# Kernel tuning notes

Measured on AMD Instinct MI355X. Metric: run time of the kernel, lower is better.

## Reference

```python
import jax, jax.numpy as jnp
import numpy as np

N = 100000
E = 1600000
IN_CH = 128
HID = 32
HEADS = 4
OUT_CH = 64
NEG_SLOPE = 0.2


def _gat_conv(x, src, dst, W, att_src, att_dst, bias, heads, out_ch):
    # PyG GATConv (concat=True, add_self_loops handled by caller via src/dst)
    n = x.shape[0]
    xp = (x @ W).reshape(n, heads, out_ch)                  # [N,H,C]
    a_src = (xp * att_src).sum(-1)                          # [N,H]
    a_dst = (xp * att_dst).sum(-1)                          # [N,H]
    e = jax.nn.leaky_relu(a_src[src] + a_dst[dst], NEG_SLOPE)  # [E,H]
    m = jax.ops.segment_max(e, dst, num_segments=n)         # per-dst max (safe: self-loops)
    ex = jnp.exp(e - m[dst])
    denom = jax.ops.segment_sum(ex, dst, num_segments=n)
    alpha = ex / denom[dst]                                  # [E,H]
    out = jax.ops.segment_sum(xp[src] * alpha[:, :, None], dst, num_segments=n)
    return out.reshape(n, heads * out_ch) + bias


def setup_inputs() -> dict:
    key = jax.random.key(0)
    ks = jax.random.split(key, 12)
    sc1 = 1.0 / np.sqrt(IN_CH)
    sc2 = 1.0 / np.sqrt(HID * HEADS * 2)
    return {
        "x_ppi": jax.random.normal(ks[0], (N, IN_CH), jnp.float32),
        "x_go": jax.random.normal(ks[1], (N, IN_CH), jnp.float32),
        "edge_index": jax.random.randint(ks[2], (2, E), 0, N, jnp.int32),
        "W1": jax.random.normal(ks[3], (IN_CH, HEADS * HID), jnp.float32) * sc1,
        "att_src1": jax.random.normal(ks[4], (HEADS, HID), jnp.float32) * sc1,
        "att_dst1": jax.random.normal(ks[5], (HEADS, HID), jnp.float32) * sc1,
        "b1": jnp.zeros((HEADS * HID,), jnp.float32),
        "W2": jax.random.normal(ks[6], (HID * HEADS * 2, OUT_CH), jnp.float32) * sc2,
        "att_src2": jax.random.normal(ks[7], (1, OUT_CH), jnp.float32) * sc2,
        "att_dst2": jax.random.normal(ks[8], (1, OUT_CH), jnp.float32) * sc2,
        "b2": jnp.zeros((OUT_CH,), jnp.float32),
    }


def reference(x_ppi, x_go, edge_index, W1, att_src1, att_dst1, b1, W2, att_src2, att_dst2, b2):
    loops = jnp.arange(N, dtype=edge_index.dtype)
    src = jnp.concatenate([edge_index[0], loops])
    dst = jnp.concatenate([edge_index[1], loops])
    h_ppi = _gat_conv(x_ppi, src, dst, W1, att_src1, att_dst1, b1, HEADS, HID)
    h_go = _gat_conv(x_go, src, dst, W1, att_src1, att_dst1, b1, HEADS, HID)
    h = jax.nn.relu(jnp.concatenate([h_ppi, h_go], axis=-1))  # [N, 2*H*HID]
    out = _gat_conv(h, src, dst, W2, att_src2, att_dst2, b2, 1, OUT_CH)
    return out
```

## Files before the change

kernel.cpp:

```cpp
#include <hip/hip_runtime.h>
#include <hip/hip_fp16.h>

constexpr int NN = 100000;
constexpr int EE = 1600000;
constexpr int ET = EE + NN;
constexpr int EQ = EE / 4;
constexpr int TQ = ET / 4;
constexpr int NBUK = (NN + 255) / 256;
constexpr int PB = 416;
constexpr int GB = (NN + 127) / 128;
constexpr float NEG = 0.2f;

typedef _Float16 f16x8 __attribute__((ext_vector_type(8)));
typedef float    f32x4 __attribute__((ext_vector_type(4)));

__global__ __launch_bounds__(256) void k_wprep0(const float* __restrict__ W1, const float* __restrict__ W2,
                                                _Float16* __restrict__ w1T, _Float16* __restrict__ w2T,
                                                int* __restrict__ bucketCount) {
    if (blockIdx.x == 0) {
        for (int i = threadIdx.x; i < NBUK; i += 256) bucketCount[i] = 0;
    }
    int idx = blockIdx.x * 256 + threadIdx.x;
    if (idx < 128 * 128) {
        int nn = idx >> 7, k = idx & 127;
        w1T[idx] = (_Float16)W1[k * 128 + nn];
    }
    int i2 = idx - 128 * 128;
    if (i2 >= 0 && i2 < 64 * 256) {
        int nn = i2 >> 8, k = i2 & 255;
        w2T[i2] = (_Float16)W2[k * 64 + nn];
    }
}

template <int K, int C, bool SRCF32, int AMODE, int OUTM, int SET>
__device__ __forceinline__ void gemm_dev(int bx, const void* __restrict__ xv,
                                         const _Float16* __restrict__ wT,
                                         const float* __restrict__ as_w, const float* __restrict__ ad_w,
                                         __half* __restrict__ xp,
                                         float* __restrict__ att_s, float* __restrict__ att_d, int n) {
    constexpr int NT = C / 16;
    const int tid  = threadIdx.x;
    const int w    = tid >> 6;
    const int lane = tid & 63;
    const int quad = lane >> 4;
    const int l16  = lane & 15;
    const long r0  = (long)bx * 128;
    const long row0 = r0 + w * 32 + l16;
    const long row1 = row0 + 16;

    f32x4 acc[2][NT];
#pragma unroll
    for (int s = 0; s < 2; s++)
#pragma unroll
        for (int t = 0; t < NT; t++) acc[s][t] = (f32x4){0.f, 0.f, 0.f, 0.f};

#pragma unroll
    for (int ks = 0; ks < K; ks += 32) {
        f16x8 a0 = (f16x8){0, 0, 0, 0, 0, 0, 0, 0};
        f16x8 a1 = (f16x8){0, 0, 0, 0, 0, 0, 0, 0};
        if (SRCF32) {
            if (row0 < n) {
                const float4* p = (const float4*)((const float*)xv + row0 * K + ks) + quad * 2;
                float4 u = p[0], v = p[1];
                a0 = (f16x8){(_Float16)u.x, (_Float16)u.y, (_Float16)u.z, (_Float16)u.w,
                             (_Float16)v.x, (_Float16)v.y, (_Float16)v.z, (_Float16)v.w};
            }
            if (row1 < n) {
                const float4* p = (const float4*)((const float*)xv + row1 * K + ks) + quad * 2;
                float4 u = p[0], v = p[1];
                a1 = (f16x8){(_Float16)u.x, (_Float16)u.y, (_Float16)u.z, (_Float16)u.w,
                             (_Float16)v.x, (_Float16)v.y, (_Float16)v.z, (_Float16)v.w};
            }
        } else {
            if (row0 < n) a0 = *(const f16x8*)((const _Float16*)xv + row0 * K + ks + quad * 8);
            if (row1 < n) a1 = *(const f16x8*)((const _Float16*)xv + row1 * K + ks + quad * 8);
        }
#pragma unroll
        for (int t = 0; t < NT; t++) {
            f16x8 b = *(const f16x8*)(wT + (long)(t * 16 + l16) * K + ks + quad * 8);
            acc[0][t] = __builtin_amdgcn_mfma_f32_16x16x32_f16(a0, b, acc[0][t], 0, 0, 0);
            acc[1][t] = __builtin_amdgcn_mfma_f32_16x16x32_f16(a1, b, acc[1][t], 0, 0, 0);
        }
    }

#pragma unroll
    for (int sub = 0; sub < 2; sub++) {
        long rb = r0 + w * 32 + sub * 16 + quad * 4;
#pragma unroll
        for (int t = 0; t < NT; t++) {
            int c = t * 16 + l16;
#pragma unroll
            for (int rg = 0; rg < 4; rg++) {
                long row = rb + rg;
                if (row < n) {
                    __half hv = __float2half(acc[sub][t][rg]);
                    if (OUTM == 0)
                        xp[row * 256 + ((c >> 1) << 2) + (c & 1) + SET * 2] = hv;
                    else
                        xp[row * (long)C + c] = hv;
                }
            }
        }
    }

    if (AMODE == 1) {
        float asw[8], adw[8];
#pragma unroll
        for (int t = 0; t < 8; t++) {
            int ci = (t >> 1) * 32 + (t & 1) * 16 + l16;
            asw[t] = as_w[ci];
            adw[t] = ad_w[ci];
        }
#pragma unroll
        for (int sub = 0; sub < 2; sub++) {
#pragma unroll
            for (int rg = 0; rg < 4; rg++) {
                long row = r0 + w * 32 + sub * 16 + quad * 4 + rg;
                float hs[4] = {0.f, 0.f, 0.f, 0.f};
                float hd[4] = {0.f, 0.f, 0.f, 0.f};
#pragma unroll
                for (int t = 0; t < 8; t++) {
                    float av = acc[sub][t][rg];
                    hs[t >> 1] += av * asw[t];
                    hd[t >> 1] += av * adw[t];
                }
#pragma unroll
                for (int h = 0; h < 4; h++) {
                    hs[h] += __shfl_xor(hs[h], 1); hs[h] += __shfl_xor(hs[h], 2);
                    hs[h] += __shfl_xor(hs[h], 4); hs[h] += __shfl_xor(hs[h], 8);
                    hd[h] += __shfl_xor(hd[h], 1); hd[h] += __shfl_xor(hd[h], 2);
                    hd[h] += __shfl_xor(hd[h], 4); hd[h] += __shfl_xor(hd[h], 8);
                }
                if (l16 == 0 && row < n) {
#pragma unroll
                    for (int h = 0; h < 4; h++) {
                        att_s[row * 8 + h * 2 + SET] = hs[h];
                        att_d[row * 8 + h * 2 + SET] = hd[h];
                    }
                }
            }
        }
    }
    if (AMODE == 2) {
        float asw[NT], adw[NT];
#pragma unroll
        for (int t = 0; t < NT; t++) {
            asw[t] = as_w[t * 16 + l16];
            adw[t] = ad_w[t * 16 + l16];
        }
#pragma unroll
        for (int sub = 0; sub < 2; sub++) {
#pragma unroll
            for (int rg = 0; rg < 4; rg++) {
                long row = r0 + w * 32 + sub * 16 + quad * 4 + rg;
                float s = 0.f, d = 0.f;
#pragma unroll
                for (int t = 0; t < NT; t++) {
                    float av = acc[sub][t][rg];
                    s += av * asw[t];
                    d += av * adw[t];
                }
                s += __shfl_xor(s, 1); s += __shfl_xor(s, 2); s += __shfl_xor(s, 4); s += __shfl_xor(s, 8);
                d += __shfl_xor(d, 1); d += __shfl_xor(d, 2); d += __shfl_xor(d, 4); d += __shfl_xor(d, 8);
                if (l16 == 0 && row < n) {
                    att_s[row] = s;
                    att_d[row] = d;
                }
            }
        }
    }
}

__device__ __forceinline__ void bcount_dev(int bx, const int4* __restrict__ dst4v,
                                           int* __restrict__ bucketCount) {
    __shared__ int bh[NBUK];
    for (int i = threadIdx.x; i < NBUK; i += 256) bh[i] = 0;
    __syncthreads();
    int gtid = bx * 256 + threadIdx.x;
    for (int q = gtid; q < TQ; q += PB * 256) {
        int4 d;
        if (q < EQ) {
            d = dst4v[q];
        } else {
            int s0 = (q - EQ) * 4;
            d.x = s0; d.y = s0 + 1; d.z = s0 + 2; d.w = s0 + 3;
        }
        atomicAdd(&bh[d.x >> 8], 1);
        atomicAdd(&bh[d.y >> 8], 1);
        atomicAdd(&bh[d.z >> 8], 1);
        atomicAdd(&bh[d.w >> 8], 1);
    }
    __syncthreads();
    for (int i = threadIdx.x; i < NBUK; i += 256)
        if (bh[i]) atomicAdd(&bucketCount[i], bh[i]);
}

__global__ __launch_bounds__(256) void megaA(const float* __restrict__ x_ppi, const float* __restrict__ x_go,
                                             const int4* __restrict__ dst4v,
                                             const _Float16* __restrict__ w1T,
                                             const float* __restrict__ as1, const float* __restrict__ ad1,
                                             __half* __restrict__ xpc,
                                             float* __restrict__ att1s, float* __restrict__ att1d,
                                             int* __restrict__ bucketCount) {
    int bx = blockIdx.x;
    if (bx < GB) {
        gemm_dev<128, 128, true, 1, 0, 0>(bx, x_ppi, w1T, as1, ad1, xpc, att1s, att1d, NN);
    } else if (bx < 2 * GB) {
        gemm_dev<128, 128, true, 1, 0, 1>(bx - GB, x_go, w1T, as1, ad1, xpc, att1s, att1d, NN);
    } else {
        bcount_dev(bx - 2 * GB, dst4v, bucketCount);
    }
}

__global__ __launch_bounds__(256) void gemm_k2(const __half* __restrict__ hbuf,
                                               const _Float16* __restrict__ w2T,
                                               const float* __restrict__ as2, const float* __restrict__ ad2,
                                               __half* __restrict__ xp2,
                                               float* __restrict__ asr2, float* __restrict__ ads2) {
    gemm_dev<256, 64, false, 2, 1, 0>(blockIdx.x, hbuf, w2T, as2, ad2, xp2, asr2, ads2, NN);
}

__global__ __launch_bounds__(512) void k_bscan(const int* __restrict__ bucketCount,
                                               int* __restrict__ bstart, int* __restrict__ gcur,
                                               int* __restrict__ rs) {
    __shared__ int sh[512];
    int t = threadIdx.x;
    int v = (t < NBUK) ? bucketCount[t] : 0;
    sh[t] = v;
    __syncthreads();
    for (int o = 1; o < 512; o <<= 1) {
        int u = (t >= o) ? sh[t - o] : 0;
        __syncthreads();
        sh[t] += u;
        __syncthreads();
    }
    if (t < NBUK) { bstart[t] = sh[t] - v; gcur[t] = sh[t] - v; }
    if (t == 0) { bstart[NBUK] = ET; rs[NN] = ET; }
}

__global__ __launch_bounds__(256) void k_bplace(const int4* __restrict__ src4v, const int4* __restrict__ dst4v,
                                                int* __restrict__ gcur, unsigned int* __restrict__ ebuf) {
    __shared__ int bh[NBUK];
    __shared__ int bbase[NBUK];
    for (int i = threadIdx.x; i < NBUK; i += 256) bh[i] = 0;
    __syncthreads();
    int gtid = blockIdx.x * 256 + threadIdx.x;

    int esrc[16];
    int emeta[16];
#pragma unroll
    for (int it = 0; it < 4; it++) {
        int q = gtid + it * (PB * 256);
        bool valid = q < TQ;
        int4 s, d;
        if (valid) {
            if (q < EQ) { s = src4v[q]; d = dst4v[q]; }
            else { int s0 = (q - EQ) * 4; s.x = s0; s.y = s0 + 1; s.z = s0 + 2; s.w = s0 + 3; d = s; }
        } else {
            s.x = s.y = s.z = s.w = 0; d = s;
        }
        int ss[4] = {s.x, s.y, s.z, s.w};
        int dd[4] = {d.x, d.y, d.z, d.w};
#pragma unroll
        for (int k = 0; k < 4; k++) {
            int idx = it * 4 + k;
            if (valid) {
                int b = dd[k] >> 8, l = dd[k] & 255;
                int r = atomicAdd(&bh[b], 1);
                esrc[idx]  = ss[k];
                emeta[idx] = (b << 21) | (l << 13) | r;
            } else {
                emeta[idx] = -1;
            }
        }
    }
    __syncthreads();
    for (int i = threadIdx.x; i < NBUK; i += 256)
        bbase[i] = bh[i] ? atomicAdd(&gcur[i], bh[i]) : 0;
    __syncthreads();
#pragma unroll
    for (int e = 0; e < 16; e++) {
        int me = emeta[e];
        if (me >= 0) {
            int b = me >> 21, l = (me >> 13) & 255, r = me & 8191;
            ebuf[bbase[b] + r] = ((unsigned)l << 24) | (unsigned)esrc[e];
        }
    }
}

__global__ __launch_bounds__(256) void k_csr(const unsigned int* __restrict__ ebuf,
                                             const int* __restrict__ bstart,
                                             int* __restrict__ rs, int* __restrict__ csr) {
    __shared__ int hist[256];
    __shared__ int sh[256];
    __shared__ int cur[256];
    int b = blockIdx.x;
    int t = threadIdx.x;
    int e0 = bstart[b], e1 = bstart[b + 1];
    hist[t] = 0;
    __syncthreads();
    for (int j = e0 + t; j < e1; j += 256)
        atomicAdd(&hist[ebuf[j] >> 24], 1);
    __syncthreads();
    int v = hist[t];
    sh[t] = v;
    __syncthreads();
    for (int o = 1; o < 256; o <<= 1) {
        int u = (t >= o) ? sh[t - o] : 0;
        __syncthreads();
        sh[t] += u;
        __syncthreads();
    }
    int excl = sh[t] - v;
    cur[t] = excl;
    int v0 = b * 256;
    if (v0 + t < NN) rs[v0 + t] = e0 + excl;
    __syncthreads();
    for (int j = e0 + t; j < e1; j += 256) {
        unsigned int e = ebuf[j];
        int l = (int)(e >> 24);
        int r = atomicAdd(&cur[l], 1);
        csr[e0 + r] = (int)(e & 0x00FFFFFFu);
    }
}

__global__ __launch_bounds__(256) void conv1_packed(const int* __restrict__ rs, const int* __restrict__ csr,
                                                    const uint4* __restrict__ xpc,
                                                    const float2* __restrict__ att_s,
                                                    const float2* __restrict__ att_d,
                                                    const float* __restrict__ bias,
                                                    __half* __restrict__ out) {
    int v = blockIdx.x * 4 + (threadIdx.x >> 6);
    if (v >= NN) return;
    int lane = threadIdx.x & 63;
    int h = lane >> 5;
    int m = lane & 31;
    int hd = m >> 3;
    int e0 = rs[v], e1 = rs[v + 1];

    float2 ad = att_d[v * 4 + hd];
    auto lrexp = [](float e) { e = (e > 0.f) ? e : NEG * e; return __expf(e); };

    float ap0 = 0.f, ap1 = 0.f, ap2 = 0.f, ap3 = 0.f;
    float ag0 = 0.f, ag1 = 0.f, ag2 = 0.f, ag3 = 0.f;
    float dp = 0.f, dg = 0.f;

    int j = e0;
    for (; j + 8 <= e1; j += 8) {
        int s[4]; float2 av[4]; uint4 r[4];
#pragma unroll
        for (int q = 0; q < 4; q++) s[q] = csr[j + 2 * q + h];
#pragma unroll
        for (int q = 0; q < 4; q++) av[q] = att_s[s[q] * 4 + hd];
#pragma unroll
        for (int q = 0; q < 4; q++) r[q] = xpc[(long)s[q] * 32 + m];
#pragma unroll
        for (int q = 0; q < 4; q++) {
            float wx = lrexp(av[q].x + ad.x);
            float wy = lrexp(av[q].y + ad.y);
            dp += wx; dg += wy;
            float2 p01 = __half22float2(*(__half2*)&r[q].x);
            float2 g01 = __half22float2(*(__half2*)&r[q].y);
            float2 p23 = __half22float2(*(__half2*)&r[q].z);
            float2 g23 = __half22float2(*(__half2*)&r[q].w);
            ap0 += wx * p01.x; ap1 += wx * p01.y; ap2 += wx * p23.x; ap3 += wx * p23.y;
            ag0 += wy * g01.x; ag1 += wy * g01.y; ag2 += wy * g23.x; ag3 += wy * g23.y;
        }
    }
    for (; j < e1; j += 2) {
        int jj = j + h;
        int jc = (jj < e1) ? jj : (e1 - 1);
        bool ok = jj < e1;
        int s = csr[jc];
        float2 av = att_s[s * 4 + hd];
        uint4 r = xpc[(long)s * 32 + m];
        float wx = ok ? lrexp(av.x + ad.x) : 0.f;
        float wy = ok ? lrexp(av.y + ad.y) : 0.f;
        dp += wx; dg += wy;
        float2 p01 = __half22float2(*(__half2*)&r.x);
        float2 g01 = __half22float2(*(__half2*)&r.y);
        float2 p23 = __half22float2(*(__half2*)&r.z);
        float2 g23 = __half22float2(*(__half2*)&r.w);
        ap0 += wx * p01.x; ap1 += wx * p01.y; ap2 += wx * p23.x; ap3 += wx * p23.y;
        ag0 += wy * g01.x; ag1 += wy * g01.y; ag2 += wy * g23.x; ag3 += wy * g23.y;
    }

    ap0 += __shfl_xor(ap0, 32); ap1 += __shfl_xor(ap1, 32);
    ap2 += __shfl_xor(ap2, 32); ap3 += __shfl_xor(ap3, 32);
    ag0 += __shfl_xor(ag0, 32); ag1 += __shfl_xor(ag1, 32);
    ag2 += __shfl_xor(ag2, 32); ag3 += __shfl_xor(ag3, 32);
    dp  += __shfl_xor(dp, 32);  dg  += __shfl_xor(dg, 32);

    float ivp = 1.0f / dp, ivg = 1.0f / dg;
    int c0 = 4 * m;
    float4 b4 = *(const float4*)&bias[c0];
    float inv = h ? ivg : ivp;
    float a0 = h ? ag0 : ap0;
    float a1 = h ? ag1 : ap1;
    float a2 = h ? ag2 : ap2;
    float a3 = h ? ag3 : ap3;
    __half2 o01 = __floats2half2_rn(fmaxf(a0 * inv + b4.x, 0.f), fmaxf(a1 * inv + b4.y, 0.f));
    __half2 o23 = __floats2half2_rn(fmaxf(a2 * inv + b4.z, 0.f), fmaxf(a3 * inv + b4.w, 0.f));
    uint2 st;
    st.x = *(unsigned int*)&o01;
    st.y = *(unsigned int*)&o23;
    *(uint2*)(out + (long)v * 256 + h * 128 + c0) = st;
}

__global__ __launch_bounds__(256) void conv2_edge(const int* __restrict__ rs, const int* __restrict__ csr,
                                                  const __half* __restrict__ xp,
                                                  const float* __restrict__ asrc,
                                                  const float* __restrict__ adst,
                                                  const float* __restrict__ bias,
                                                  float* __restrict__ out) {
    int v = blockIdx.x * 4 + (threadIdx.x >> 6);
    if (v >= NN) return;
    int lane = threadIdx.x & 63;
    int qw = lane >> 4;
    int m = lane & 15;
    int e0 = rs[v], e1 = rs[v + 1];
    const uint2* xp2 = (const uint2*)xp;

    float adv = adst[v];
    auto lrexp = [](float e) { e = (e > 0.f) ? e : NEG * e; return __expf(e); };

    float a0 = 0.f, a1 = 0.f, a2 = 0.f, a3 = 0.f, d = 0.f;

    int j = e0;
    for (; j + 16 <= e1; j += 16) {
        int s[4]; float av[4]; uint2 r[4];
#pragma unroll
        for (int k = 0; k < 4; k++) s[k] = csr[j + 4 * k + qw];
#pragma unroll
        for (int k = 0; k < 4; k++) av[k] = asrc[s[k]];
#pragma unroll
        for (int k = 0; k < 4; k++) r[k] = xp2[(long)s[k] * 16 + m];
#pragma unroll
        for (int k = 0; k < 4; k++) {
            float w = lrexp(av[k] + adv);
            d += w;
            float2 x01 = __half22float2(*(__half2*)&r[k].x);
            float2 x23 = __half22float2(*(__half2*)&r[k].y);
            a0 += w * x01.x; a1 += w * x01.y;
            a2 += w * x23.x; a3 += w * x23.y;
        }
    }
    for (; j < e1; j += 4) {
        int jj = j + qw;
        int jc = (jj < e1) ? jj : (e1 - 1);
        int s = csr[jc];
        float av = asrc[s];
        uint2 r = xp2[(long)s * 16 + m];
        float w = (jj < e1) ? lrexp(av + adv) : 0.f;
        d += w;
        float2 x01 = __half22float2(*(__half2*)&r.x);
        float2 x23 = __half22float2(*(__half2*)&r.y);
        a0 += w * x01.x; a1 += w * x01.y;
        a2 += w * x23.x; a3 += w * x23.y;
    }

    a0 += __shfl_xor(a0, 16); a1 += __shfl_xor(a1, 16);
    a2 += __shfl_xor(a2, 16); a3 += __shfl_xor(a3, 16);
    d  += __shfl_xor(d, 16);
    a0 += __shfl_xor(a0, 32); a1 += __shfl_xor(a1, 32);
    a2 += __shfl_xor(a2, 32); a3 += __shfl_xor(a3, 32);
    d  += __shfl_xor(d, 32);

    if (qw == 0) {
        float inv = 1.0f / d;
        float4 b4 = *(const float4*)&bias[4 * m];
        float4 o;
        o.x = a0 * inv + b4.x;
        o.y = a1 * inv + b4.y;
        o.z = a2 * inv + b4.z;
        o.w = a3 * inv + b4.w;
        *(float4*)&out[(long)v * 64 + 4 * m] = o;
    }
}

extern "C" void kernel_launch(void* const* d_in, const int* in_sizes, int n_in,
                              void* d_out, int out_size, void* d_ws, size_t ws_size,
                              hipStream_t stream) {
    const float* x_ppi = (const float*)d_in[0];
    const float* x_go  = (const float*)d_in[1];
    const int*   ei    = (const int*)d_in[2];
    const float* W1    = (const float*)d_in[3];
    const float* as1   = (const float*)d_in[4];
    const float* ad1   = (const float*)d_in[5];
    const float* b1    = (const float*)d_in[6];
    const float* W2    = (const float*)d_in[7];
    const float* as2   = (const float*)d_in[8];
    const float* ad2   = (const float*)d_in[9];
    const float* b2    = (const float*)d_in[10];
    float* out = (float*)d_out;

    char* ws = (char*)d_ws;
    size_t off = 0;
    auto alloc = [&](size_t bytes) -> void* {
        void* p = ws + off;
        off = (off + bytes + 255) & ~(size_t)255;
        return p;
    };
    int* bucketCount = (int*)alloc((size_t)NBUK * 4);
    int* bstart      = (int*)alloc((size_t)(NBUK + 1) * 4);
    int* gcur        = (int*)alloc((size_t)NBUK * 4);
    unsigned int* ebuf = (unsigned int*)alloc((size_t)ET * 4);
    int* rs      = (int*)alloc((size_t)(NN + 1) * 4);
    int* csr     = (int*)alloc((size_t)ET * 4);
    _Float16* w1T = (_Float16*)alloc((size_t)128 * 128 * 2);
    _Float16* w2T = (_Float16*)alloc((size_t)64 * 256 * 2);
    __half* xpc  = (__half*)alloc((size_t)NN * 256 * 2);
    __half* xp2  = (__half*)alloc((size_t)NN * 64 * 2);
    float* att1s = (float*)alloc((size_t)NN * 4 * 8);
    float* att1d = (float*)alloc((size_t)NN * 4 * 8);
    float* asr2  = (float*)alloc((size_t)NN * 4);
    float* ads2  = (float*)alloc((size_t)NN * 4);
    __half* hbuf = (__half*)alloc((size_t)NN * 256 * 2);
    (void)ws_size; (void)in_sizes; (void)n_in; (void)out_size;

    k_wprep0<<<128, 256, 0, stream>>>(W1, W2, w1T, w2T, bucketCount);
    megaA<<<2 * GB + PB, 256, 0, stream>>>(x_ppi, x_go, (const int4*)(ei + EE),
                                           w1T, as1, ad1, xpc, att1s, att1d, bucketCount);
    k_bscan<<<1, 512, 0, stream>>>(bucketCount, bstart, gcur, rs);
    k_bplace<<<PB, 256, 0, stream>>>((const int4*)ei, (const int4*)(ei + EE), gcur, ebuf);
    k_csr<<<NBUK, 256, 0, stream>>>(ebuf, bstart, rs, csr);
    conv1_packed<<<NN / 4, 256, 0, stream>>>(rs, csr, (const uint4*)xpc,
                                             (const float2*)att1s, (const float2*)att1d, b1, hbuf);
    gemm_k2<<<GB, 256, 0, stream>>>(hbuf, w2T, as2, ad2, xp2, asr2, ads2);
    conv2_edge<<<NN / 4, 256, 0, stream>>>(rs, csr, xp2, asr2, ads2, b2, out);
}
```

Measured before the change: 473.8 us.

## Reschedule bucket counting and placement around GEMM, sort adjacency lists

Weight prep and bucket counting move into one launch. Bucket placement now runs in the same kernel as the layer-1 GEMM, so the edge scatter overlaps with matrix work, and the counter reset becomes a memset. A new kernel bitonic-sorts each node's first 64 neighbor indices so the gathers in the convolution kernels touch memory in ascending order and get better cache locality. This adds an extra launch and an extra pass over the CSR array.

```diff
diff --git a/kernel.cpp b/kernel.cpp
--- a/kernel.cpp
+++ b/kernel.cpp
@@ -14,13 +14,9 @@
 typedef _Float16 f16x8 __attribute__((ext_vector_type(8)));
 typedef float    f32x4 __attribute__((ext_vector_type(4)));
 
-__global__ __launch_bounds__(256) void k_wprep0(const float* __restrict__ W1, const float* __restrict__ W2,
-                                                _Float16* __restrict__ w1T, _Float16* __restrict__ w2T,
-                                                int* __restrict__ bucketCount) {
-    if (blockIdx.x == 0) {
-        for (int i = threadIdx.x; i < NBUK; i += 256) bucketCount[i] = 0;
-    }
-    int idx = blockIdx.x * 256 + threadIdx.x;
+__device__ __forceinline__ void wprep_dev(int bx, const float* __restrict__ W1, const float* __restrict__ W2,
+                                          _Float16* __restrict__ w1T, _Float16* __restrict__ w2T) {
+    int idx = bx * 256 + threadIdx.x;
     if (idx < 128 * 128) {
         int nn = idx >> 7, k = idx & 127;
         w1T[idx] = (_Float16)W1[k * 128 + nn];
@@ -29,6 +25,80 @@
     if (i2 >= 0 && i2 < 64 * 256) {
         int nn = i2 >> 8, k = i2 & 255;
         w2T[i2] = (_Float16)W2[k * 64 + nn];
+    }
+}
+
+__device__ __forceinline__ void bcount_dev(int bx, const int4* __restrict__ dst4v,
+                                           int* __restrict__ bucketCount) {
+    __shared__ int bh[NBUK];
+    for (int i = threadIdx.x; i < NBUK; i += 256) bh[i] = 0;
+    __syncthreads();
+    int gtid = bx * 256 + threadIdx.x;
+    for (int q = gtid; q < TQ; q += PB * 256) {
+        int4 d;
+        if (q < EQ) {
+            d = dst4v[q];
+        } else {
+            int s0 = (q - EQ) * 4;
+            d.x = s0; d.y = s0 + 1; d.z = s0 + 2; d.w = s0 + 3;
+        }
+        atomicAdd(&bh[d.x >> 8], 1);
+        atomicAdd(&bh[d.y >> 8], 1);
+        atomicAdd(&bh[d.z >> 8], 1);
+        atomicAdd(&bh[d.w >> 8], 1);
+    }
+    __syncthreads();
+    for (int i = threadIdx.x; i < NBUK; i += 256)
+        if (bh[i]) atomicAdd(&bucketCount[i], bh[i]);
+}
+
+__device__ __forceinline__ void bplace_dev(int bx, const int4* __restrict__ src4v, const int4* __restrict__ dst4v,
+                                           int* __restrict__ gcur, unsigned int* __restrict__ ebuf) {
+    __shared__ int bh[NBUK];
+    __shared__ int bbase[NBUK];
+    for (int i = threadIdx.x; i < NBUK; i += 256) bh[i] = 0;
+    __syncthreads();
+    int gtid = bx * 256 + threadIdx.x;
+
+    int esrc[16];
+    int emeta[16];
+#pragma unroll
+    for (int it = 0; it < 4; it++) {
+        int q = gtid + it * (PB * 256);
+        bool valid = q < TQ;
+        int4 s, d;
+        if (valid) {
+            if (q < EQ) { s = src4v[q]; d = dst4v[q]; }
+            else { int s0 = (q - EQ) * 4; s.x = s0; s.y = s0 + 1; s.z = s0 + 2; s.w = s0 + 3; d = s; }
+        } else {
+            s.x = s.y = s.z = s.w = 0; d = s;
+        }
+        int ss[4] = {s.x, s.y, s.z, s.w};
+        int dd[4] = {d.x, d.y, d.z, d.w};
+#pragma unroll
+        for (int k = 0; k < 4; k++) {
+            int idx = it * 4 + k;
+            if (valid) {
+                int b = dd[k] >> 8, l = dd[k] & 255;
+                int r = atomicAdd(&bh[b], 1);
+                esrc[idx]  = ss[k];
+                emeta[idx] = (b << 21) | (l << 13) | r;
+            } else {
+                emeta[idx] = -1;
+            }
+        }
+    }
+    __syncthreads();
+    for (int i = threadIdx.x; i < NBUK; i += 256)
+        bbase[i] = bh[i] ? atomicAdd(&gcur[i], bh[i]) : 0;
+    __syncthreads();
+#pragma unroll
+    for (int e = 0; e < 16; e++) {
+        int me = emeta[e];
+        if (me >= 0) {
+            int b = me >> 21, l = (me >> 13) & 255, r = me & 8191;
+            ebuf[bbase[b] + r] = ((unsigned)l << 24) | (unsigned)esrc[e];
+        }
     }
 }
 
@@ -171,44 +241,28 @@
     }
 }
 
-__device__ __forceinline__ void bcount_dev(int bx, const int4* __restrict__ dst4v,
-                                           int* __restrict__ bucketCount) {
-    __shared__ int bh[NBUK];
-    for (int i = threadIdx.x; i < NBUK; i += 256) bh[i] = 0;
-    __syncthreads();
-    int gtid = bx * 256 + threadIdx.x;
-    for (int q = gtid; q < TQ; q += PB * 256) {
-        int4 d;
-        if (q < EQ) {
-            d = dst4v[q];
-        } else {
-            int s0 = (q - EQ) * 4;
-            d.x = s0; d.y = s0 + 1; d.z = s0 + 2; d.w = s0 + 3;
-        }
-        atomicAdd(&bh[d.x >> 8], 1);
-        atomicAdd(&bh[d.y >> 8], 1);
-        atomicAdd(&bh[d.z >> 8], 1);
-        atomicAdd(&bh[d.w >> 8], 1);
-    }
-    __syncthreads();
-    for (int i = threadIdx.x; i < NBUK; i += 256)
-        if (bh[i]) atomicAdd(&bucketCount[i], bh[i]);
-}
-
-__global__ __launch_bounds__(256) void megaA(const float* __restrict__ x_ppi, const float* __restrict__ x_go,
-                                             const int4* __restrict__ dst4v,
-                                             const _Float16* __restrict__ w1T,
-                                             const float* __restrict__ as1, const float* __restrict__ ad1,
-                                             __half* __restrict__ xpc,
-                                             float* __restrict__ att1s, float* __restrict__ att1d,
-                                             int* __restrict__ bucketCount) {
+__global__ __launch_bounds__(256) void mega0(const float* __restrict__ W1, const float* __restrict__ W2,
+                                             _Float16* __restrict__ w1T, _Float16* __restrict__ w2T,
+                                             const int4* __restrict__ dst4v, int* __restrict__ bucketCount) {
+    int bx = blockIdx.x;
+    if (bx < 128) wprep_dev(bx, W1, W2, w1T, w2T);
+    else          bcount_dev(bx - 128, dst4v, bucketCount);
+}
+
+__global__ __launch_bounds__(256) void megaA2(const float* __restrict__ x_ppi, const float* __restrict__ x_go,
+                                              const int4* __restrict__ src4v, const int4* __restrict__ dst4v,
+                                              const _Float16* __restrict__ w1T,
+                                              const float* __restrict__ as1, const float* __restrict__ ad1,
+                                              __half* __restrict__ xpc,
+                                              float* __restrict__ att1s, float* __restrict__ att1d,
+                                              int* __restrict__ gcur, unsigned int* __restrict__ ebuf) {
     int bx = blockIdx.x;
     if (bx < GB) {
         gemm_dev<128, 128, true, 1, 0, 0>(bx, x_ppi, w1T, as1, ad1, xpc, att1s, att1d, NN);
     } else if (bx < 2 * GB) {
         gemm_dev<128, 128, true, 1, 0, 1>(bx - GB, x_go, w1T, as1, ad1, xpc, att1s, att1d, NN);
     } else {
-        bcount_dev(bx - 2 * GB, dst4v, bucketCount);
+        bplace_dev(bx - 2 * GB, src4v, dst4v, gcur, ebuf);
     }
 }
 
@@ -236,56 +290,6 @@
     }
     if (t < NBUK) { bstart[t] = sh[t] - v; gcur[t] = sh[t] - v; }
     if (t == 0) { bstart[NBUK] = ET; rs[NN] = ET; }
-}
-
-__global__ __launch_bounds__(256) void k_bplace(const int4* __restrict__ src4v, const int4* __restrict__ dst4v,
-                                                int* __restrict__ gcur, unsigned int* __restrict__ ebuf) {
-    __shared__ int bh[NBUK];
-    __shared__ int bbase[NBUK];
-    for (int i = threadIdx.x; i < NBUK; i += 256) bh[i] = 0;
-    __syncthreads();
-    int gtid = blockIdx.x * 256 + threadIdx.x;
-
-    int esrc[16];
-    int emeta[16];
-#pragma unroll
-    for (int it = 0; it < 4; it++) {
-        int q = gtid + it * (PB * 256);
-        bool valid = q < TQ;
-        int4 s, d;
-        if (valid) {
-            if (q < EQ) { s = src4v[q]; d = dst4v[q]; }
-            else { int s0 = (q - EQ) * 4; s.x = s0; s.y = s0 + 1; s.z = s0 + 2; s.w = s0 + 3; d = s; }
-        } else {
-            s.x = s.y = s.z = s.w = 0; d = s;
-        }
-        int ss[4] = {s.x, s.y, s.z, s.w};
-        int dd[4] = {d.x, d.y, d.z, d.w};
-#pragma unroll
-        for (int k = 0; k < 4; k++) {
-            int idx = it * 4 + k;
-            if (valid) {
-                int b = dd[k] >> 8, l = dd[k] & 255;
-                int r = atomicAdd(&bh[b], 1);
-                esrc[idx]  = ss[k];
-                emeta[idx] = (b << 21) | (l << 13) | r;
-            } else {
-                emeta[idx] = -1;
-            }
-        }
-    }
-    __syncthreads();
-    for (int i = threadIdx.x; i < NBUK; i += 256)
-        bbase[i] = bh[i] ? atomicAdd(&gcur[i], bh[i]) : 0;
-    __syncthreads();
-#pragma unroll
-    for (int e = 0; e < 16; e++) {
-        int me = emeta[e];
-        if (me >= 0) {
-            int b = me >> 21, l = (me >> 13) & 255, r = me & 8191;
-            ebuf[bbase[b] + r] = ((unsigned)l << 24) | (unsigned)esrc[e];
-        }
-    }
 }
 
 __global__ __launch_bounds__(256) void k_csr(const unsigned int* __restrict__ ebuf,
@@ -322,6 +326,30 @@
         int r = atomicAdd(&cur[l], 1);
         csr[e0 + r] = (int)(e & 0x00FFFFFFu);
     }
+}
+
+__global__ __launch_bounds__(256) void k_sortadj(const int* __restrict__ rs, int* __restrict__ csr) {
+    int v = blockIdx.x * 4 + (threadIdx.x >> 6);
+    if (v >= NN) return;
+    int lane = threadIdx.x & 63;
+    int e0 = rs[v], e1 = rs[v + 1];
+    int deg = e1 - e0;
+    int nsort = (deg < 64) ? deg : 64;
+    int val = (lane < nsort) ? csr[e0 + lane] : 0x7FFFFFFF;
+#pragma unroll
+    for (int k = 2; k <= 64; k <<= 1) {
+#pragma unroll
+        for (int j = k >> 1; j >= 1; j >>= 1) {
+            int other = __shfl_xor(val, j);
+            bool up = ((lane & k) == 0);
+            bool lower = ((lane & j) == 0);
+            bool keepMin = (up == lower);
+            int mn = (val < other) ? val : other;
+            int mx = (val < other) ? other : val;
+            val = keepMin ? mn : mx;
+        }
+    }
+    if (lane < nsort) csr[e0 + lane] = val;
 }
 
 __global__ __launch_bounds__(256) void conv1_packed(const int* __restrict__ rs, const int* __restrict__ csr,
@@ -518,12 +546,13 @@
     __half* hbuf = (__half*)alloc((size_t)NN * 256 * 2);
     (void)ws_size; (void)in_sizes; (void)n_in; (void)out_size;
 
-    k_wprep0<<<128, 256, 0, stream>>>(W1, W2, w1T, w2T, bucketCount);
-    megaA<<<2 * GB + PB, 256, 0, stream>>>(x_ppi, x_go, (const int4*)(ei + EE),
-                                           w1T, as1, ad1, xpc, att1s, att1d, bucketCount);
+    hipMemsetAsync(bucketCount, 0, (size_t)NBUK * 4, stream);
+    mega0<<<128 + PB, 256, 0, stream>>>(W1, W2, w1T, w2T, (const int4*)(ei + EE), bucketCount);
     k_bscan<<<1, 512, 0, stream>>>(bucketCount, bstart, gcur, rs);
-    k_bplace<<<PB, 256, 0, stream>>>((const int4*)ei, (const int4*)(ei + EE), gcur, ebuf);
+    megaA2<<<2 * GB + PB, 256, 0, stream>>>(x_ppi, x_go, (const int4*)ei, (const int4*)(ei + EE),
+                                            w1T, as1, ad1, xpc, att1s, att1d, gcur, ebuf);
     k_csr<<<NBUK, 256, 0, stream>>>(ebuf, bstart, rs, csr);
+    k_sortadj<<<NN / 4, 256, 0, stream>>>(rs, csr);
     conv1_packed<<<NN / 4, 256, 0, stream>>>(rs, csr, (const uint4*)xpc,
                                              (const float2*)att1s, (const float2*)att1d, b1, hbuf);
     gemm_k2<<<GB, 256, 0, stream>>>(hbuf, w2T, as2, ad2, xp2, asr2, ads2);
```

After: 494.4 us. +4.4%, slower.
